# Performance work log

Hardware: AMD Instinct MI355X
Metric: run time of the kernel (lower is better)

Reference implementation:

```python
import jax, jax.numpy as jnp
import numpy as np

B, L, D_MODEL = 2, 2048, 2048
D_INNER, D_STATE, D_CONV, DT_RANK = 4096, 16, 4, 128


def setup_inputs() -> dict:
    key = jax.random.key(0)
    ks = jax.random.split(key, 8)
    s = 0.02
    return {
        "hidden_states": jax.random.normal(ks[0], (B, L, D_MODEL), jnp.float32),
        "in_proj_weight": jax.random.normal(ks[1], (2 * D_INNER, D_MODEL), jnp.float32) * s,
        "conv1d_weight": jax.random.normal(ks[2], (D_INNER, 1, D_CONV), jnp.float32) * s,
        "conv1d_bias": jnp.zeros((D_INNER,), jnp.float32),
        "x_proj_weight": jax.random.normal(ks[3], (DT_RANK + 2 * D_STATE, D_INNER), jnp.float32) * s,
        "dt_proj_weight": jax.random.normal(ks[4], (D_INNER, DT_RANK), jnp.float32) * s,
        "dt_proj_bias": jax.random.uniform(ks[5], (D_INNER,), jnp.float32, -4.0, -2.0),
        "out_proj_weight": jax.random.normal(ks[6], (D_MODEL, D_INNER), jnp.float32) * s,
        # real Mamba init: A_log = log(1..d_state) broadcast over channels
        "A_log": jnp.log(jnp.broadcast_to(jnp.arange(1, D_STATE + 1, dtype=jnp.float32), (D_INNER, D_STATE))),
        "D": jnp.ones((D_INNER,), jnp.float32),
    }


def reference(hidden_states, in_proj_weight, conv1d_weight, conv1d_bias,
              x_proj_weight, dt_proj_weight, dt_proj_bias, out_proj_weight,
              A_log, D):
    negA = -jnp.exp(A_log)  # [d_inner, d_state]
    # in_proj (no bias) then transpose(1,2): [B, 2*d_inner, L]
    xz = jnp.einsum('bld,ed->bel', hidden_states, in_proj_weight)
    x, z = jnp.split(xz, 2, axis=1)  # each [B, d_inner, L]
    # causal depthwise conv1d + silu
    x = jax.lax.conv_general_dilated(
        x, conv1d_weight, window_strides=(1,), padding=[(D_CONV - 1, 0)],
        dimension_numbers=('NCH', 'OIH', 'NCH'), feature_group_count=D_INNER,
    ) + conv1d_bias[None, :, None]
    x = jax.nn.silu(x)
    xT = x.transpose(0, 2, 1)  # [B, L, d_inner]
    # x_proj -> (dt_rank, d_state, d_state)
    x_dbl = jnp.einsum('bld,ed->ble', xT, x_proj_weight)
    dt_lo = x_dbl[..., :DT_RANK]
    Bm = x_dbl[..., DT_RANK:DT_RANK + D_STATE]   # [B, L, n]
    Cm = x_dbl[..., DT_RANK + D_STATE:]          # [B, L, n]
    # dt_proj + delta_bias, softplus (delta_softplus=True)
    dt = jax.nn.softplus(jnp.einsum('blr,dr->bld', dt_lo, dt_proj_weight) + dt_proj_bias)

    # selective scan: h_t = exp(dt_t*A)*h_{t-1} + dt_t*x_t*B_t ; y_t = C_t . h_t
    def step(h, inp):
        dt_t, B_t, C_t, x_t = inp  # [B,d],[B,n],[B,n],[B,d]
        dA = jnp.exp(dt_t[..., None] * negA)           # [B, d, n]
        h = h * dA + (dt_t * x_t)[..., None] * B_t[:, None, :]
        y = jnp.einsum('bdn,bn->bd', h, C_t)
        return h, y

    h0 = jnp.zeros((B, D_INNER, D_STATE), dt.dtype)
    _, ys = jax.lax.scan(
        step, h0,
        (dt.transpose(1, 0, 2), Bm.transpose(1, 0, 2),
         Cm.transpose(1, 0, 2), xT.transpose(1, 0, 2)),
    )  # ys: [L, B, d_inner]
    y = ys.transpose(1, 0, 2) + xT * D          # skip connection D*x
    y = y * jax.nn.silu(z.transpose(0, 2, 1))   # gate
    # out_proj (no bias): [B, L, d_model]
    return jnp.einsum('bld,ed->ble', y, out_proj_weight)
```

## Files before the change

kernel.cpp:

```cpp
#include <hip/hip_runtime.h>
#include <math.h>

#define B_ 2
#define L_ 2048
#define DMODEL 2048
#define DINNER 4096
#define DSTATE 16
#define DCONV 4
#define DTRANK 128
#define NCHUNK 32
#define CLEN 64
#define MROWS 4096

typedef unsigned short ushort_t;
typedef unsigned int uint_t;
typedef __attribute__((ext_vector_type(8))) short bf16x8;
typedef __attribute__((ext_vector_type(4))) float floatx4;

__device__ __forceinline__ float sigmoidf_(float x){ return 1.f/(1.f+__expf(-x)); }
__device__ __forceinline__ ushort_t f2bf(float f){
    uint_t u = __builtin_bit_cast(uint_t, f);
    return (ushort_t)((u + 0x7FFFu + ((u >> 16) & 1u)) >> 16);
}
__device__ __forceinline__ float bf2f(ushort_t h){
    return __builtin_bit_cast(float, (uint_t)h << 16);
}
__device__ __forceinline__ float fast_exp2(float x){
#if __has_builtin(__builtin_amdgcn_exp2f)
    return __builtin_amdgcn_exp2f(x);
#else
    return exp2f(x);
#endif
}
#define LOG2E 1.44269504088896f

#define GLD_LDS16(g, l) __builtin_amdgcn_global_load_lds( \
    (const __attribute__((address_space(1))) void*)(g),   \
    (__attribute__((address_space(3))) void*)(l), 16, 0, 0)

template<int OUTBF, int EPI, int SPLIT, int KSPLIT>
__global__ __launch_bounds__(256)
void gemm_mfma(const ushort_t* __restrict__ Aptr, int lda,
               const ushort_t* __restrict__ W, int ldw,
               void* __restrict__ Cptr, void* __restrict__ C2,
               int ldc, int Klen,
               const float* __restrict__ bias)
{
    __shared__ ushort_t lsA[128*64];
    __shared__ ushort_t lsW[128*64];
    const int tid  = threadIdx.x;
    const int row0 = blockIdx.x * 128;
    const int col0 = blockIdx.y * 128;
    const int koff = KSPLIT ? blockIdx.z * Klen : 0;
    const int lane = tid & 63;
    const int wv   = tid >> 6;
    const int wm   = (wv >> 1) * 64;
    const int wn   = (wv & 1) * 64;
    const int lr   = lane & 15;
    const int lq   = lane >> 4;

    floatx4 acc[4][4];
    #pragma unroll
    for(int i=0;i<4;i++)
        #pragma unroll
        for(int j=0;j<4;j++)
            #pragma unroll
            for(int r=0;r<4;r++) acc[i][j][r] = 0.f;

    for(int k0 = koff; k0 < koff + Klen; k0 += 64){
        #pragma unroll
        for(int it=0; it<4; it++){
            const int slot = it*256 + tid;
            const int row  = slot >> 3;
            const int p    = slot & 7;
            const int s    = p ^ (row & 7);
            const ushort_t* gw = W    + (size_t)(col0 + row)*ldw + k0 + s*8;
            const ushort_t* ga = Aptr + (size_t)(row0 + row)*lda + k0 + s*8;
            GLD_LDS16(gw, &lsW[slot*8]);
            GLD_LDS16(ga, &lsA[slot*8]);
        }
        __syncthreads();

        #pragma unroll
        for(int kk=0; kk<2; kk++){
            bf16x8 af[4], bw[4];
            #pragma unroll
            for(int i=0;i<4;i++){
                const int ra = wm + i*16 + lr;
                const int rb = wn + i*16 + lr;
                af[i] = *(const bf16x8*)&lsA[ra*64 + (((kk*4+lq) ^ (ra&7))*8)];
                bw[i] = *(const bf16x8*)&lsW[rb*64 + (((kk*4+lq) ^ (rb&7))*8)];
            }
            #pragma unroll
            for(int i=0;i<4;i++)
                #pragma unroll
                for(int j=0;j<4;j++)
                    acc[i][j] = __builtin_amdgcn_mfma_f32_16x16x32_bf16(af[i], bw[j], acc[i][j], 0, 0, 0);
        }
        __syncthreads();
    }

    void* dst = Cptr;
    int cbase = col0;
    if (SPLIT && col0 >= ldc){ dst = C2; cbase = col0 - ldc; }
    const size_t zoff = KSPLIT ? (size_t)blockIdx.z * MROWS * ldc : 0;

    #pragma unroll
    for(int i=0;i<4;i++){
        #pragma unroll
        for(int r=0;r<4;r++){
            const int row = row0 + wm + i*16 + lq*4 + r;
            #pragma unroll
            for(int j=0;j<4;j++){
                const int col = cbase + wn + j*16 + lr;
                float v = acc[i][j][r];
                if (EPI){
                    v += bias[col];
                    v = (v > 20.f) ? v : log1pf(expf(v));
                }
                if (OUTBF) ((ushort_t*)dst)[(size_t)row*ldc + col] = f2bf(v);
                else       ((float*)  dst)[zoff + (size_t)row*ldc + col] = v;
            }
        }
    }
}

template<int OUTBF, int SPLIT, int KSPLIT>
__global__ __launch_bounds__(512, 2)
void gemm_256(const ushort_t* __restrict__ Aptr, int lda,
              const ushort_t* __restrict__ W, int ldw,
              void* __restrict__ Cptr, void* __restrict__ C2,
              int ldc, int Klen)
{
    __shared__ ushort_t lds[2][2][2][8192];
    const int tid  = threadIdx.x;
    const int row0 = blockIdx.x * 256;
    const int col0 = blockIdx.y * 256;
    const int koff = KSPLIT ? blockIdx.z * Klen : 0;
    const int NT   = Klen >> 6;
    const int lane = tid & 63;
    const int wv   = tid >> 6;
    const int wr   = wv >> 2;
    const int wc   = wv & 3;
    const int lr   = lane & 15;
    const int lq   = lane >> 4;

    int sdst0, sdst1;
    const ushort_t *aS0, *aS1, *wS0, *wS1;
    {
        const int g0 = tid,     dr0 = g0 >> 3, f0 = g0 & 7;
        const int g1 = 512+tid, dr1 = g1 >> 3, f1 = g1 & 7;
        const int u0 = f0 ^ (dr0 & 7), u1 = f1 ^ (dr1 & 7);
        const int r0s = dr0*2 + (u0 >> 2), c0s = (u0 & 3)*8;
        const int r1s = dr1*2 + (u1 >> 2), c1s = (u1 & 3)*8;
        sdst0 = g0*8; sdst1 = g1*8;
        aS0 = Aptr + (size_t)(row0 + r0s)*lda + c0s;
        aS1 = Aptr + (size_t)(row0 + r1s)*lda + c1s;
        wS0 = W    + (size_t)(col0 + r0s)*ldw + c0s;
        wS1 = W    + (size_t)(col0 + r1s)*ldw + c1s;
    }
    #define STG_A(kc, reg) { GLD_LDS16(aS0 + (kc), &(reg)[sdst0]); \
                             GLD_LDS16(aS1 + (kc), &(reg)[sdst1]); }
    #define STG_W(kc, reg) { GLD_LDS16(wS0 + (kc), &(reg)[sdst0]); \
                             GLD_LDS16(wS1 + (kc), &(reg)[sdst1]); }

    const int frd = ((lr & 1)*4 + lq) ^ (lr >> 1);
    const int aA  = (wr*64 + (lr >> 1))*64 + frd*8;
    const int aB  = (wc*32 + (lr >> 1))*64 + frd*8;

    floatx4 acc[8][4];
    #pragma unroll
    for(int i=0;i<8;i++)
        #pragma unroll
        for(int j=0;j<4;j++)
            #pragma unroll
            for(int r=0;r<4;r++) acc[i][j][r] = 0.f;

    STG_A(koff,    lds[0][0][0]);
    STG_W(koff,    lds[0][1][0]);
    STG_A(koff+32, lds[0][0][1]);
    STG_W(koff+32, lds[0][1][1]);
    STG_A(koff+64, lds[1][0][0]);
    STG_W(koff+64, lds[1][1][0]);
    asm volatile("s_waitcnt vmcnt(8)\ns_barrier" ::: "memory");

    for(int t=0; t<NT; ++t){
        const int c = t & 1;
        const ushort_t* LA0 = lds[c][0][0];
        const ushort_t* LB0 = lds[c][1][0];
        const ushort_t* LA1 = lds[c][0][1];
        const ushort_t* LB1 = lds[c][1][1];
        const int kt1 = koff + (t+1)*64;
        const int kt2 = koff + (t+2)*64;
        bf16x8 af[8], b0, b1;

        #pragma unroll
        for(int i=0;i<8;i++) af[i] = *(const bf16x8*)&LA0[aA + i*512];
        b0 = *(const bf16x8*)&LB0[aB];
        b1 = *(const bf16x8*)&LB0[aB + 512];
        if (t+1 < NT) STG_A(kt1+32, lds[c^1][0][1]);
        __builtin_amdgcn_s_barrier();
        asm volatile("s_waitcnt lgkmcnt(0)" ::: "memory");
        __builtin_amdgcn_s_setprio(1);
        #pragma unroll
        for(int i=0;i<8;i++){
            acc[i][0] = __builtin_amdgcn_mfma_f32_16x16x32_bf16(af[i], b0, acc[i][0],0,0,0);
            acc[i][1] = __builtin_amdgcn_mfma_f32_16x16x32_bf16(af[i], b1, acc[i][1],0,0,0);
        }
        __builtin_amdgcn_s_setprio(0);
        __builtin_amdgcn_s_barrier();

        b0 = *(const bf16x8*)&LB0[aB + 1024];
        b1 = *(const bf16x8*)&LB0[aB + 1536];
        if (t+1 < NT) STG_W(kt1+32, lds[c^1][1][1]);
        __builtin_amdgcn_s_barrier();
        asm volatile("s_waitcnt lgkmcnt(0)" ::: "memory");
        __builtin_amdgcn_s_setprio(1);
        #pragma unroll
        for(int i=0;i<8;i++){
            acc[i][2] = __builtin_amdgcn_mfma_f32_16x16x32_bf16(af[i], b0, acc[i][2],0,0,0);
            acc[i][3] = __builtin_amdgcn_mfma_f32_16x16x32_bf16(af[i], b1, acc[i][3],0,0,0);
        }
        __builtin_amdgcn_s_setprio(0);
        if (t+1 < NT) asm volatile("s_waitcnt vmcnt(8)\ns_barrier" ::: "memory");
        else          asm volatile("s_waitcnt vmcnt(0)\ns_barrier" ::: "memory");

        #pragma unroll
        for(int i=0;i<8;i++) af[i] = *(const bf16x8*)&LA1[aA + i*512];
        b0 = *(const bf16x8*)&LB1[aB];
        b1 = *(const bf16x8*)&LB1[aB + 512];
        if (t+2 < NT) STG_A(kt2, lds[c][0][0]);
        __builtin_amdgcn_s_barrier();
        asm volatile("s_waitcnt lgkmcnt(0)" ::: "memory");
        __builtin_amdgcn_s_setprio(1);
        #pragma unroll
        for(int i=0;i<8;i++){
            acc[i][0] = __builtin_amdgcn_mfma_f32_16x16x32_bf16(af[i], b0, acc[i][0],0,0,0);
            acc[i][1] = __builtin_amdgcn_mfma_f32_16x16x32_bf16(af[i], b1, acc[i][1],0,0,0);
        }
        __builtin_amdgcn_s_setprio(0);
        __builtin_amdgcn_s_barrier();

        b0 = *(const bf16x8*)&LB1[aB + 1024];
        b1 = *(const bf16x8*)&LB1[aB + 1536];
        if (t+2 < NT) STG_W(kt2, lds[c][1][0]);
        __builtin_amdgcn_s_barrier();
        asm volatile("s_waitcnt lgkmcnt(0)" ::: "memory");
        __builtin_amdgcn_s_setprio(1);
        #pragma unroll
        for(int i=0;i<8;i++){
            acc[i][2] = __builtin_amdgcn_mfma_f32_16x16x32_bf16(af[i], b0, acc[i][2],0,0,0);
            acc[i][3] = __builtin_amdgcn_mfma_f32_16x16x32_bf16(af[i], b1, acc[i][3],0,0,0);
        }
        __builtin_amdgcn_s_setprio(0);
        if (t+2 < NT)      asm volatile("s_waitcnt vmcnt(8)\ns_barrier" ::: "memory");
        else if (t+1 < NT) asm volatile("s_waitcnt vmcnt(4)\ns_barrier" ::: "memory");
        else               asm volatile("s_barrier" ::: "memory");
    }
    #undef STG_A
    #undef STG_W

    void* dst = Cptr;
    int cb = col0;
    if (SPLIT && col0 >= ldc){ dst = C2; cb = col0 - ldc; }
    const size_t zoff = KSPLIT ? (size_t)blockIdx.z * MROWS * ldc : 0;
    const int rbase = row0 + wr*128 + lq*4;
    const int cbase = cb + wc*64 + lr;
    #pragma unroll
    for(int i=0;i<8;i++){
        #pragma unroll
        for(int r=0;r<4;r++){
            const int row = rbase + i*16 + r;
            #pragma unroll
            for(int j=0;j<4;j++){
                const int col = cbase + j*16;
                const float v = acc[i][j][r];
                if (OUTBF) ((ushort_t*)dst)[(size_t)row*ldc + col] = f2bf(v);
                else       ((float*)dst)[zoff + (size_t)row*ldc + col] = v;
            }
        }
    }
}

__global__ __launch_bounds__(256)
void reduce2(const float* __restrict__ P, float* __restrict__ out, int n4)
{
    const int i = blockIdx.x*256 + threadIdx.x;
    if (i < n4){
        float4 a = *(const float4*)(P + (size_t)i*4);
        float4 b = *(const float4*)(P + (size_t)(i + n4)*4);
        float4 r; r.x=a.x+b.x; r.y=a.y+b.y; r.z=a.z+b.z; r.w=a.w+b.w;
        *(float4*)(out + (size_t)i*4) = r;
    }
}

__global__ __launch_bounds__(256)
void cvt_bf16(const float* __restrict__ in, ushort_t* __restrict__ out, int n4)
{
    const int i = blockIdx.x*256 + threadIdx.x;
    if (i < n4){
        float4 v = *(const float4*)(in + (size_t)i*4);
        union { ushort_t u[4]; uint2 q; } p;
        p.u[0]=f2bf(v.x); p.u[1]=f2bf(v.y); p.u[2]=f2bf(v.z); p.u[3]=f2bf(v.w);
        *(uint2*)(out + (size_t)i*4) = p.q;
    }
}

__global__ __launch_bounds__(256)
void cvt_pad256(const float* __restrict__ in, ushort_t* __restrict__ out)
{
    const int i = blockIdx.x*256 + threadIdx.x;
    const int row = i >> 10;
    const int c4  = i & 1023;
    union { ushort_t u[4]; uint2 q; } p;
    if (row < 160){
        float4 v = *(const float4*)(in + (size_t)row*4096 + c4*4);
        p.u[0]=f2bf(v.x); p.u[1]=f2bf(v.y); p.u[2]=f2bf(v.z); p.u[3]=f2bf(v.w);
    } else { p.u[0]=0; p.u[1]=0; p.u[2]=0; p.u[3]=0; }
    *(uint2*)(out + (size_t)i*4) = p.q;
}

__global__ __launch_bounds__(256)
void reduce_xproj(const float* __restrict__ P, float* __restrict__ xdbl,
                  ushort_t* __restrict__ dtlo)
{
    const int row = blockIdx.x;
    const int col = threadIdx.x;
    float s = 0.f;
    #pragma unroll
    for(int z=0; z<8; z++)
        s += P[(size_t)z*MROWS*256 + (size_t)row*256 + col];
    if (col < 160) xdbl[(size_t)row*160 + col] = s;
    if (col < DTRANK) dtlo[(size_t)row*DTRANK + col] = f2bf(s);
}

__global__ __launch_bounds__(256)
void conv_silu_bf(const ushort_t* __restrict__ xb, const float* __restrict__ w,
                  const float* __restrict__ bias, ushort_t* __restrict__ xc)
{
    const int gid = blockIdx.x*256 + threadIdx.x;
    const int d = gid & (DINNER-1);
    const int t = gid >> 12;
    const int l = t & (L_-1);
    float s = bias[d];
    #pragma unroll
    for(int j=0;j<DCONV;j++){
        const int ll = l - (DCONV-1) + j;
        if (ll >= 0)
            s = fmaf(bf2f(xb[(size_t)(t-(DCONV-1)+j)*DINNER + d]), w[d*DCONV+j], s);
    }
    xc[(size_t)t*DINNER + d] = f2bf(s * sigmoidf_(s));
}

__global__ __launch_bounds__(256)
void scan_phase1(const ushort_t* __restrict__ dt_bf,
                 const ushort_t* __restrict__ xconv,
                 const float* __restrict__ xdbl,
                 const float* __restrict__ A_log,
                 float* __restrict__ sc_h, float* __restrict__ sc_S)
{
    const int tid = threadIdx.x;
    const int d = blockIdx.x*256 + tid;
    const int chunk = blockIdx.y;
    const int b = blockIdx.z;
    const int l0 = chunk*CLEN;

    __shared__ float Bs[CLEN][DSTATE];
    for(int i=tid; i<CLEN*DSTATE; i+=256){
        const int row = i >> 4, n = i & 15;
        Bs[row][n] = xdbl[(size_t)(b*L_ + l0 + row)*160 + DTRANK + n];
    }
    float negA[DSTATE];
    #pragma unroll
    for(int n=0;n<DSTATE;n++) negA[n] = -expf(A_log[d*DSTATE + n]) * LOG2E;
    __syncthreads();

    float h[DSTATE], S[DSTATE];
    #pragma unroll
    for(int n=0;n<DSTATE;n++){ h[n]=0.f; S[n]=0.f; }

    size_t idx = (size_t)(b*L_ + l0)*DINNER + d;
    float dt_c = bf2f(dt_bf[idx]);
    float xv_c = bf2f(xconv[idx]);
    for(int l=0;l<CLEN;l++){
        float dt_n = 0.f, xv_n = 0.f;
        if (l+1 < CLEN){
            dt_n = bf2f(dt_bf[idx + DINNER]);
            xv_n = bf2f(xconv[idx + DINNER]);
        }
        const float dx = dt_c * xv_c;
        #pragma unroll
        for(int n=0;n<DSTATE;n++){
            const float t = dt_c * negA[n];
            S[n] += t;
            h[n] = fmaf(h[n], fast_exp2(t), dx*Bs[l][n]);
        }
        dt_c = dt_n; xv_c = xv_n;
        idx += DINNER;
    }
    const size_t o = (size_t)(b*NCHUNK + chunk)*DSTATE*DINNER + d;
    #pragma unroll
    for(int n=0;n<DSTATE;n++){
        sc_h[o + (size_t)n*DINNER] = h[n];
        sc_S[o + (size_t)n*DINNER] = S[n];
    }
}

__global__ __launch_bounds__(256)
void scan_phase2(float* __restrict__ sc_h, const float* __restrict__ sc_S)
{
    const int gid = blockIdx.x*256 + threadIdx.x;
    const int b = gid / (DSTATE*DINNER);
    const int rem = gid - b*DSTATE*DINNER;
    const size_t base = (size_t)b*NCHUNK*DSTATE*DINNER + rem;
    float H = 0.f;
    #pragma unroll
    for(int c=0;c<NCHUNK;c++){
        const size_t idx = base + (size_t)c*DSTATE*DINNER;
        const float he = sc_h[idx];
        const float S  = sc_S[idx];
        sc_h[idx] = H;
        H = fmaf(fast_exp2(S), H, he);
    }
}

__global__ __launch_bounds__(256)
void scan_phase3(const ushort_t* __restrict__ dt_bf,
                 const ushort_t* __restrict__ xconv,
                 const float* __restrict__ xdbl,
                 const ushort_t* __restrict__ z_bf,
                 const float* __restrict__ A_log,
                 const float* __restrict__ Dvec,
                 const float* __restrict__ sc_h,
                 ushort_t* __restrict__ y_bf)
{
    const int tid = threadIdx.x;
    const int d = blockIdx.x*256 + tid;
    const int chunk = blockIdx.y;
    const int b = blockIdx.z;
    const int l0 = chunk*CLEN;

    __shared__ float BCs[CLEN][2*DSTATE];
    for(int i=tid; i<CLEN*2*DSTATE; i+=256){
        const int row = i >> 5, c = i & 31;
        BCs[row][c] = xdbl[(size_t)(b*L_ + l0 + row)*160 + DTRANK + c];
    }
    float negA[DSTATE];
    #pragma unroll
    for(int n=0;n<DSTATE;n++) negA[n] = -expf(A_log[d*DSTATE + n]) * LOG2E;
    const float Dv = Dvec[d];
    float h[DSTATE];
    const size_t o = (size_t)(b*NCHUNK + chunk)*DSTATE*DINNER + d;
    #pragma unroll
    for(int n=0;n<DSTATE;n++) h[n] = sc_h[o + (size_t)n*DINNER];
    __syncthreads();

    size_t idx = (size_t)(b*L_ + l0)*DINNER + d;
    float dt_c = bf2f(dt_bf[idx]);
    float xv_c = bf2f(xconv[idx]);
    float zv_c = bf2f(z_bf[idx]);
    for(int l=0;l<CLEN;l++){
        float dt_n = 0.f, xv_n = 0.f, zv_n = 0.f;
        if (l+1 < CLEN){
            dt_n = bf2f(dt_bf[idx + DINNER]);
            xv_n = bf2f(xconv[idx + DINNER]);
            zv_n = bf2f(z_bf[idx + DINNER]);
        }
        const float dx = dt_c * xv_c;
        float y = 0.f;
        #pragma unroll
        for(int n=0;n<DSTATE;n++){
            const float t = dt_c * negA[n];
            h[n] = fmaf(h[n], fast_exp2(t), dx*BCs[l][n]);
            y = fmaf(h[n], BCs[l][DSTATE+n], y);
        }
        const float g = zv_c * sigmoidf_(zv_c);
        y_bf[idx] = f2bf(fmaf(xv_c, Dv, y) * g);
        dt_c = dt_n; xv_c = xv_n; zv_c = zv_n;
        idx += DINNER;
    }
}

extern "C" void kernel_launch(void* const* d_in, const int* in_sizes, int n_in,
                              void* d_out, int out_size, void* d_ws, size_t ws_size,
                              hipStream_t stream) {
    const float* hs      = (const float*)d_in[0];
    const float* w_in    = (const float*)d_in[1];
    const float* w_conv  = (const float*)d_in[2];
    const float* b_conv  = (const float*)d_in[3];
    const float* w_xproj = (const float*)d_in[4];
    const float* w_dt    = (const float*)d_in[5];
    const float* b_dt    = (const float*)d_in[6];
    const float* w_out   = (const float*)d_in[7];
    const float* A_log   = (const float*)d_in[8];
    const float* Dvec    = (const float*)d_in[9];
    float* out = (float*)d_out;

    char* base = (char*)d_ws;
    ushort_t* x_bf   = (ushort_t*)(base);
    float*    xdbl   = (float*)   (base);
    ushort_t* wx_bf  = (ushort_t*)(base + (4u<<20));
    ushort_t* dtlo_bf= (ushort_t*)(base + (6u<<20));
    ushort_t* wdt_bf = (ushort_t*)(base + (7u<<20));
    float*    sc_h   = (float*)   (base + (8u<<20));
    ushort_t* z_bf   = (ushort_t*)(base + (32u<<20));
    float*    op_par = (float*)   (base + (32u<<20));
    ushort_t* xconv  = (ushort_t*)(base + (64u<<20));
    ushort_t* wi_bf  = (ushort_t*)(base + (96u<<20));
    ushort_t* dt_bf  = (ushort_t*)(base + (96u<<20));
    ushort_t* hs_bf  = (ushort_t*)(base + (128u<<20));
    float*    sc_S   = (float*)   (base + (128u<<20));
    ushort_t* wo_bf  = (ushort_t*)(base + (128u<<20));
    float*    xp_par = (float*)   (base + (144u<<20));
    ushort_t* y_bf   = (ushort_t*)(base + (144u<<20));

    dim3 blk(256);
    dim3 blk5(512);

    cvt_bf16<<<dim3(MROWS*DMODEL/4/256), blk, 0, stream>>>(hs, hs_bf, MROWS*DMODEL/4);
    cvt_bf16<<<dim3(2*DINNER*DMODEL/4/256), blk, 0, stream>>>(w_in, wi_bf, 2*DINNER*DMODEL/4);

    gemm_256<1,1,0><<<dim3(MROWS/256, 2*DINNER/256), blk5, 0, stream>>>(
        hs_bf, DMODEL, wi_bf, DMODEL, x_bf, z_bf, DINNER, DMODEL);

    conv_silu_bf<<<dim3((size_t)MROWS*DINNER/256), blk, 0, stream>>>(x_bf, w_conv, b_conv, xconv);

    cvt_pad256<<<dim3(256*4096/4/256), blk, 0, stream>>>(w_xproj, wx_bf);
    gemm_mfma<0,0,0,1><<<dim3(MROWS/128, 2, 8), blk, 0, stream>>>(
        xconv, DINNER, wx_bf, DINNER, xp_par, nullptr, 256, DINNER/8, nullptr);
    reduce_xproj<<<dim3(MROWS), blk, 0, stream>>>(xp_par, xdbl, dtlo_bf);

    cvt_bf16<<<dim3(DINNER*DTRANK/4/256), blk, 0, stream>>>(w_dt, wdt_bf, DINNER*DTRANK/4);
    gemm_mfma<1,1,0,0><<<dim3(MROWS/128, DINNER/128), blk, 0, stream>>>(
        dtlo_bf, DTRANK, wdt_bf, DTRANK, dt_bf, nullptr, DINNER, DTRANK, b_dt);

    dim3 sgrid(DINNER/256, NCHUNK, B_);
    scan_phase1<<<sgrid, blk, 0, stream>>>(dt_bf, xconv, xdbl, A_log, sc_h, sc_S);
    scan_phase2<<<dim3(B_*DSTATE*DINNER/256), blk, 0, stream>>>(sc_h, sc_S);

    cvt_bf16<<<dim3(DMODEL*DINNER/4/256), blk, 0, stream>>>(w_out, wo_bf, DMODEL*DINNER/4);

    scan_phase3<<<sgrid, blk, 0, stream>>>(dt_bf, xconv, xdbl, z_bf, A_log, Dvec, sc_h, y_bf);

    gemm_256<0,0,1><<<dim3(MROWS/256, DMODEL/256, 2), blk5, 0, stream>>>(
        y_bf, DINNER, wo_bf, DINNER, op_par, nullptr, DMODEL, DINNER/2);
    reduce2<<<dim3(MROWS*DMODEL/4/256), blk, 0, stream>>>(op_par, out, MROWS*DMODEL/4);
}
```

Measured before the change: 685.6 us.

## Merge gemm_256 half-k-steps into single phases; use 128-tile GEMM for out_proj

The 256x256 GEMM inner loop now issues all four B fragments and eight A fragments per half k-step and runs 32 MFMAs at once, replacing two sub-phases that each had their own barriers and waitcnts. Both global-to-LDS stages are issued together, which removes several barriers per iteration. The out_proj no longer uses split-K gemm_256 plus a reduce2 pass; it calls the 128-tile gemm_mfma directly into the output, dropping the partial-sum buffer and the extra reduction kernel. Holding all fragments live raises register pressure, and the final last-iteration barrier branch is gone, which may affect correctness of LDS reuse timing.

```diff
diff --git a/kernel.cpp b/kernel.cpp
--- a/kernel.cpp
+++ b/kernel.cpp
@@ -186,76 +186,49 @@
 
     for(int t=0; t<NT; ++t){
         const int c = t & 1;
-        const ushort_t* LA0 = lds[c][0][0];
-        const ushort_t* LB0 = lds[c][1][0];
-        const ushort_t* LA1 = lds[c][0][1];
-        const ushort_t* LB1 = lds[c][1][1];
+        const ushort_t* cA0 = lds[c][0][0];
+        const ushort_t* cB0 = lds[c][1][0];
+        const ushort_t* cA1 = lds[c][0][1];
+        const ushort_t* cB1 = lds[c][1][1];
         const int kt1 = koff + (t+1)*64;
         const int kt2 = koff + (t+2)*64;
-        bf16x8 af[8], b0, b1;
-
-        #pragma unroll
-        for(int i=0;i<8;i++) af[i] = *(const bf16x8*)&LA0[aA + i*512];
-        b0 = *(const bf16x8*)&LB0[aB];
-        b1 = *(const bf16x8*)&LB0[aB + 512];
-        if (t+1 < NT) STG_A(kt1+32, lds[c^1][0][1]);
-        __builtin_amdgcn_s_barrier();
-        asm volatile("s_waitcnt lgkmcnt(0)" ::: "memory");
+        bf16x8 bw[4], af[8];
+
+        #pragma unroll
+        for(int j=0;j<4;j++) bw[j] = *(const bf16x8*)&cB0[aB + j*512];
+        #pragma unroll
+        for(int i=0;i<8;i++) af[i] = *(const bf16x8*)&cA0[aA + i*512];
+        if (t+1 < NT){
+            STG_A(kt1+32, lds[c^1][0][1]);
+            STG_W(kt1+32, lds[c^1][1][1]);
+        }
         __builtin_amdgcn_s_setprio(1);
         #pragma unroll
-        for(int i=0;i<8;i++){
-            acc[i][0] = __builtin_amdgcn_mfma_f32_16x16x32_bf16(af[i], b0, acc[i][0],0,0,0);
-            acc[i][1] = __builtin_amdgcn_mfma_f32_16x16x32_bf16(af[i], b1, acc[i][1],0,0,0);
-        }
-        __builtin_amdgcn_s_setprio(0);
-        __builtin_amdgcn_s_barrier();
-
-        b0 = *(const bf16x8*)&LB0[aB + 1024];
-        b1 = *(const bf16x8*)&LB0[aB + 1536];
-        if (t+1 < NT) STG_W(kt1+32, lds[c^1][1][1]);
-        __builtin_amdgcn_s_barrier();
-        asm volatile("s_waitcnt lgkmcnt(0)" ::: "memory");
-        __builtin_amdgcn_s_setprio(1);
-        #pragma unroll
-        for(int i=0;i<8;i++){
-            acc[i][2] = __builtin_amdgcn_mfma_f32_16x16x32_bf16(af[i], b0, acc[i][2],0,0,0);
-            acc[i][3] = __builtin_amdgcn_mfma_f32_16x16x32_bf16(af[i], b1, acc[i][3],0,0,0);
-        }
+        for(int i=0;i<8;i++)
+            #pragma unroll
+            for(int j=0;j<4;j++)
+                acc[i][j] = __builtin_amdgcn_mfma_f32_16x16x32_bf16(af[i], bw[j], acc[i][j],0,0,0);
         __builtin_amdgcn_s_setprio(0);
         if (t+1 < NT) asm volatile("s_waitcnt vmcnt(8)\ns_barrier" ::: "memory");
         else          asm volatile("s_waitcnt vmcnt(0)\ns_barrier" ::: "memory");
 
         #pragma unroll
-        for(int i=0;i<8;i++) af[i] = *(const bf16x8*)&LA1[aA + i*512];
-        b0 = *(const bf16x8*)&LB1[aB];
-        b1 = *(const bf16x8*)&LB1[aB + 512];
-        if (t+2 < NT) STG_A(kt2, lds[c][0][0]);
-        __builtin_amdgcn_s_barrier();
-        asm volatile("s_waitcnt lgkmcnt(0)" ::: "memory");
+        for(int j=0;j<4;j++) bw[j] = *(const bf16x8*)&cB1[aB + j*512];
+        #pragma unroll
+        for(int i=0;i<8;i++) af[i] = *(const bf16x8*)&cA1[aA + i*512];
+        if (t+2 < NT){
+            STG_A(kt2, lds[c][0][0]);
+            STG_W(kt2, lds[c][1][0]);
+        }
         __builtin_amdgcn_s_setprio(1);
         #pragma unroll
-        for(int i=0;i<8;i++){
-            acc[i][0] = __builtin_amdgcn_mfma_f32_16x16x32_bf16(af[i], b0, acc[i][0],0,0,0);
-            acc[i][1] = __builtin_amdgcn_mfma_f32_16x16x32_bf16(af[i], b1, acc[i][1],0,0,0);
-        }
-        __builtin_amdgcn_s_setprio(0);
-        __builtin_amdgcn_s_barrier();
-
-        b0 = *(const bf16x8*)&LB1[aB + 1024];
-        b1 = *(const bf16x8*)&LB1[aB + 1536];
-        if (t+2 < NT) STG_W(kt2, lds[c][1][0]);
-        __builtin_amdgcn_s_barrier();
-        asm volatile("s_waitcnt lgkmcnt(0)" ::: "memory");
-        __builtin_amdgcn_s_setprio(1);
-        #pragma unroll
-        for(int i=0;i<8;i++){
-            acc[i][2] = __builtin_amdgcn_mfma_f32_16x16x32_bf16(af[i], b0, acc[i][2],0,0,0);
-            acc[i][3] = __builtin_amdgcn_mfma_f32_16x16x32_bf16(af[i], b1, acc[i][3],0,0,0);
-        }
+        for(int i=0;i<8;i++)
+            #pragma unroll
+            for(int j=0;j<4;j++)
+                acc[i][j] = __builtin_amdgcn_mfma_f32_16x16x32_bf16(af[i], bw[j], acc[i][j],0,0,0);
         __builtin_amdgcn_s_setprio(0);
         if (t+2 < NT)      asm volatile("s_waitcnt vmcnt(8)\ns_barrier" ::: "memory");
         else if (t+1 < NT) asm volatile("s_waitcnt vmcnt(4)\ns_barrier" ::: "memory");
-        else               asm volatile("s_barrier" ::: "memory");
     }
     #undef STG_A
     #undef STG_W
@@ -279,18 +252,6 @@
                 else       ((float*)dst)[zoff + (size_t)row*ldc + col] = v;
             }
         }
-    }
-}
-
-__global__ __launch_bounds__(256)
-void reduce2(const float* __restrict__ P, float* __restrict__ out, int n4)
-{
-    const int i = blockIdx.x*256 + threadIdx.x;
-    if (i < n4){
-        float4 a = *(const float4*)(P + (size_t)i*4);
-        float4 b = *(const float4*)(P + (size_t)(i + n4)*4);
-        float4 r; r.x=a.x+b.x; r.y=a.y+b.y; r.z=a.z+b.z; r.w=a.w+b.w;
-        *(float4*)(out + (size_t)i*4) = r;
     }
 }
 
@@ -504,7 +465,6 @@
     ushort_t* wdt_bf = (ushort_t*)(base + (7u<<20));
     float*    sc_h   = (float*)   (base + (8u<<20));
     ushort_t* z_bf   = (ushort_t*)(base + (32u<<20));
-    float*    op_par = (float*)   (base + (32u<<20));
     ushort_t* xconv  = (ushort_t*)(base + (64u<<20));
     ushort_t* wi_bf  = (ushort_t*)(base + (96u<<20));
     ushort_t* dt_bf  = (ushort_t*)(base + (96u<<20));
@@ -542,7 +502,6 @@
 
     scan_phase3<<<sgrid, blk, 0, stream>>>(dt_bf, xconv, xdbl, z_bf, A_log, Dvec, sc_h, y_bf);
 
-    gemm_256<0,0,1><<<dim3(MROWS/256, DMODEL/256, 2), blk5, 0, stream>>>(
-        y_bf, DINNER, wo_bf, DINNER, op_par, nullptr, DMODEL, DINNER/2);
-    reduce2<<<dim3(MROWS*DMODEL/4/256), blk, 0, stream>>>(op_par, out, MROWS*DMODEL/4);
-}
+    gemm_mfma<0,0,0,0><<<dim3(MROWS/128, DMODEL/128), blk, 0, stream>>>(
+        y_bf, DINNER, wo_bf, DINNER, out, nullptr, DMODEL, DINNER, nullptr);
+}
```

Measured after the change: 669.8 us. 2.3% less time.
